# Optimization experiments

Measured on AMD Instinct MI355X. Metric: run time of the kernel, lower is better.

Reference implementation:

```python
import jax, jax.numpy as jnp
import numpy as np

B = 1024      # batch
DIN = 103     # generator/encoder input dim
L1, L2 = 64, 32   # encoder layer widths (latent = 32)
E = 8         # NUM_EXPERTS
GH = 64       # gating hidden width
H = 256       # generator hidden width
DOUT = 51     # generator output dim
EPS = 1e-5    # BatchNorm eps


def setup_inputs() -> dict:
    key = jax.random.key(0)
    ks = jax.random.split(key, 24)
    s = 0.05
    f32 = jnp.float32
    return {
        "x": jax.random.normal(ks[0], (B, DIN), f32),
        # encoder Linear + BN params
        "w1": jax.random.normal(ks[1], (L1, DIN), f32) * s,
        "b1": jnp.zeros((L1,), f32),
        "gamma1": jnp.ones((L1,), f32),
        "beta1": jnp.zeros((L1,), f32),
        "w2": jax.random.normal(ks[2], (L2, L1), f32) * s,
        "b2": jnp.zeros((L2,), f32),
        "gamma2": jnp.ones((L2,), f32),
        "beta2": jnp.zeros((L2,), f32),
        # gating MLP (latent 32 -> GH -> GH -> E, ELU, softmax)
        "gw1": jax.random.normal(ks[3], (GH, L2), f32) * s,
        "gb1": jnp.zeros((GH,), f32),
        "gw2": jax.random.normal(ks[4], (GH, GH), f32) * s,
        "gb2": jnp.zeros((GH,), f32),
        "gw3": jax.random.normal(ks[5], (E, GH), f32) * s,
        "gb3": jnp.zeros((E,), f32),
        # expert weight banks for 3-layer generator (MANN style)
        "ew1": jax.random.normal(ks[6], (E, DIN, H), f32) * s,
        "eb1": jnp.zeros((E, H), f32),
        "ew2": jax.random.normal(ks[7], (E, H, H), f32) * s,
        "eb2": jnp.zeros((E, H), f32),
        "ew3": jax.random.normal(ks[8], (E, H, DOUT), f32) * s,
        "eb3": jnp.zeros((E, DOUT), f32),
    }


def _batchnorm(h, gamma, beta):
    # training-mode BatchNorm1d: per-batch mean/var (biased var, matching torch)
    m = jnp.mean(h, axis=0)
    v = jnp.mean((h - m) ** 2, axis=0)
    return gamma * (h - m) * jax.lax.rsqrt(v + EPS) + beta


def reference(x, w1, b1, gamma1, beta1, w2, b2, gamma2, beta2,
              gw1, gb1, gw2, gb2, gw3, gb3,
              ew1, eb1, ew2, eb2, ew3, eb3):
    # in-place scale of last 3 features (x[:,100:103] *= 100)
    xs = x.at[:, 100:103].multiply(100.0)
    # encoder: Linear -> BN -> ReLU, twice
    h = jax.nn.relu(_batchnorm(xs @ w1.T + b1, gamma1, beta1))
    latent = jax.nn.relu(_batchnorm(h @ w2.T + b2, gamma2, beta2))
    # gating network -> blending coefficients BC [B, E]
    g = jax.nn.elu(latent @ gw1.T + gb1)
    g = jax.nn.elu(g @ gw2.T + gb2)
    bc = jax.nn.softmax(g @ gw3.T + gb3, axis=-1)
    # MANN-style generator: per-sample expert-blended weights
    wb1 = jnp.einsum('be,eih->bih', bc, ew1)   # [B, DIN, H]
    h1 = jax.nn.elu(jnp.einsum('bi,bih->bh', xs, wb1) + bc @ eb1)
    wb2 = jnp.einsum('be,ehk->bhk', bc, ew2)   # [B, H, H]
    h2 = jax.nn.elu(jnp.einsum('bh,bhk->bk', h1, wb2) + bc @ eb2)
    wb3 = jnp.einsum('be,eho->bho', bc, ew3)   # [B, H, DOUT]
    out = jnp.einsum('bh,bho->bo', h2, wb3) + bc @ eb3
    return out
```

## Files before the change

### kernel.cpp

```cpp
#include <hip/hip_runtime.h>
#include <math.h>


#define DIN 103
#define L1W 64
#define L2W 32
#define NE  8
#define GH  64
#define HH  256
#define DOUT 51
#define EPSBN 1e-5f

typedef __attribute__((ext_vector_type(8))) short bf16x8;
typedef __attribute__((ext_vector_type(4))) float f32x4;
typedef __attribute__((ext_vector_type(8))) unsigned short us8;
typedef __attribute__((ext_vector_type(4))) unsigned short us4;

__device__ __forceinline__ float eluf(float v) { return v > 0.f ? v : (expf(v) - 1.f); }

__device__ __forceinline__ unsigned short bf16h(float f) {
  unsigned u = __float_as_uint(f);
  u += 0x7FFFu + ((u >> 16) & 1u);
  return (unsigned short)(u >> 16);
}
__device__ __forceinline__ float bf16f(unsigned short h) {
  return __uint_as_float(((unsigned)h) << 16);
}
__device__ __forceinline__ void split_bf16(float v, unsigned short& h, unsigned short& l) {
  h = bf16h(v);
  l = bf16h(v - bf16f(h));
}


__global__ __launch_bounds__(256) void enc_pre(const float* __restrict__ x,
    const float* __restrict__ w1, const float* __restrict__ b1,
    float* __restrict__ h1raw, float* __restrict__ stats) {
  __shared__ float w1L[DIN * L1W];
  __shared__ float lsum[L1W], lsq[L1W];
  int t = threadIdx.x;
  for (int idx = t; idx < DIN * L1W; idx += 256) w1L[idx] = w1[idx];
  if (t < L1W) { lsum[t] = 0.f; lsq[t] = 0.f; }
  __syncthreads();
  int wave = t >> 6, j = t & 63;
  int row = blockIdx.x * 4 + wave;
  const float* xr = x + row * DIN;
  float acc = b1[j];
  for (int i = 0; i < DIN; ++i) {
    float xv = xr[i];
    if (i >= 100) xv *= 100.f;
    acc = fmaf(xv, w1L[j * DIN + i], acc);
  }
  h1raw[row * L1W + j] = acc;
  atomicAdd(&lsum[j], acc);
  atomicAdd(&lsq[j], acc * acc);
  __syncthreads();
  if (t < L1W) { atomicAdd(&stats[t], lsum[t]); atomicAdd(&stats[64 + t], lsq[t]); }
}

__global__ __launch_bounds__(256) void enc_mid(const float* __restrict__ h1raw,
    const float* __restrict__ stats, const float* __restrict__ gamma1, const float* __restrict__ beta1,
    const float* __restrict__ w2, const float* __restrict__ b2,
    float* __restrict__ h2raw, float* __restrict__ stats2) {
  __shared__ float w2L[L1W * 33];
  __shared__ float sc1[L1W], sh1[L1W];
  __shared__ float ls[L2W], lq[L2W];
  int t = threadIdx.x;
  for (int idx = t; idx < L1W * L2W; idx += 256) {
    int j = idx & 31, k = idx >> 5;
    w2L[k * 33 + j] = w2[j * L1W + k];
  }
  if (t < L1W) {
    float m = stats[t] * (1.f / 1024.f);
    float v = stats[64 + t] * (1.f / 1024.f) - m * m;
    float sc = gamma1[t] * rsqrtf(v + EPSBN);
    sc1[t] = sc; sh1[t] = beta1[t] - m * sc;
  }
  if (t < L2W) { ls[t] = 0.f; lq[t] = 0.f; }
  __syncthreads();
  int wave = t >> 6, l = t & 63;
  int j = l & 31, kh = l >> 5;
  int row = blockIdx.x * 4 + wave;
  const float* hr = h1raw + row * L1W;
  float acc = 0.f;
  for (int kk = 0; kk < 32; ++kk) {
    int k = kh * 32 + kk;
    float xv = fmaxf(fmaf(hr[k], sc1[k], sh1[k]), 0.f);
    acc = fmaf(xv, w2L[k * 33 + j], acc);
  }
  float tot = acc + __shfl_xor(acc, 32);
  if (kh == 0) {
    tot += b2[j];
    h2raw[row * L2W + j] = tot;
    atomicAdd(&ls[j], tot);
    atomicAdd(&lq[j], tot * tot);
  }
  __syncthreads();
  if (t < L2W) { atomicAdd(&stats2[t], ls[t]); atomicAdd(&stats2[32 + t], lq[t]); }
}

__global__ __launch_bounds__(256) void gate_kernel(
    const float* __restrict__ h2raw, const float* __restrict__ stats2,
    const float* __restrict__ gamma2, const float* __restrict__ beta2,
    const float* __restrict__ gw1, const float* __restrict__ gb1,
    const float* __restrict__ gw2, const float* __restrict__ gb2,
    const float* __restrict__ gw3, const float* __restrict__ gb3,
    float* __restrict__ bc) {
  __shared__ float gw1L[GH * 33];
  __shared__ float gw2L[GH * 65];
  __shared__ float gw3L[NE * 65];
  __shared__ float sc2[L2W], sh2[L2W];
  __shared__ float gb1L[GH], gb2L[GH], gb3L[NE];
  __shared__ float latb[4][L2W], g1b[4][GH], g2b[4][GH], lgb[4][NE];
  int t = threadIdx.x;
  for (int idx = t; idx < GH * L2W; idx += 256) { int jj = idx >> 5, kk = idx & 31; gw1L[jj * 33 + kk] = gw1[idx]; }
  for (int idx = t; idx < GH * GH;  idx += 256) { int jj = idx >> 6, kk = idx & 63; gw2L[jj * 65 + kk] = gw2[idx]; }
  for (int idx = t; idx < NE * GH;  idx += 256) { int jj = idx >> 6, kk = idx & 63; gw3L[jj * 65 + kk] = gw3[idx]; }
  if (t < GH) { gb1L[t] = gb1[t]; gb2L[t] = gb2[t]; }
  if (t < NE) gb3L[t] = gb3[t];
  if (t < L2W) {
    float m = stats2[t] * (1.f / 1024.f);
    float v = stats2[32 + t] * (1.f / 1024.f) - m * m;
    float sc = gamma2[t] * rsqrtf(v + EPSBN);
    sc2[t] = sc; sh2[t] = beta2[t] - m * sc;
  }
  __syncthreads();
  int wave = t >> 6, l = t & 63;
  int row = blockIdx.x * 4 + wave;
  if (l < L2W) {
    float hv = h2raw[row * L2W + l];
    latb[wave][l] = fmaxf(fmaf(hv, sc2[l], sh2[l]), 0.f);
  }
  __syncthreads();
  float a1 = gb1L[l];
  for (int k = 0; k < L2W; ++k) a1 = fmaf(gw1L[l * 33 + k], latb[wave][k], a1);
  g1b[wave][l] = eluf(a1);
  __syncthreads();
  float a2 = gb2L[l];
  for (int k = 0; k < GH; ++k) a2 = fmaf(gw2L[l * 65 + k], g1b[wave][k], a2);
  g2b[wave][l] = eluf(a2);
  __syncthreads();
  if (l < NE) {
    float a3 = gb3L[l];
    for (int k = 0; k < GH; ++k) a3 = fmaf(gw3L[l * 65 + k], g2b[wave][k], a3);
    lgb[wave][l] = a3;
  }
  __syncthreads();
  if (l < NE) {
    float mx = -1e30f;
    for (int e = 0; e < NE; ++e) mx = fmaxf(mx, lgb[wave][e]);
    float sum = 0.f, mine = 0.f;
    for (int e = 0; e < NE; ++e) {
      float p = expf(lgb[wave][e] - mx);
      if (e == l) mine = p;
      sum += p;
    }
    bc[row * NE + l] = mine / sum;
  }
}


__global__ __launch_bounds__(256) void gen1(const float* __restrict__ x,
    const float* __restrict__ ew1, float* __restrict__ p) {
  __shared__ __attribute__((aligned(16))) unsigned short Ah[4096], Al[4096], Bh[4096], Bl[4096];
  int t = threadIdx.x;
  int M0 = blockIdx.x * 128, N0 = blockIdx.y * 128, e = blockIdx.z;
  int w = t >> 6, l = t & 63;
  int wm = w & 1, wn = w >> 1;
  f32x4 acc[4][4] = {};
  int ar = t >> 1, akh = (t & 1) * 16;
  int bn = t & 127, bkh = (t >> 7) * 16;
  const float* xrow = x + (size_t)(M0 + ar) * DIN;
  for (int kc = 0; kc < 4; ++kc) {
    int k0 = kc * 32;
    {
      us8 h0 = {0}, h1 = {0}, l0 = {0}, l1 = {0};
#pragma unroll
      for (int j = 0; j < 8; ++j) {
        int i = k0 + akh + j;
        float v = 0.f;
        if (i < DIN) { v = xrow[i]; if (i >= 100) v *= 100.f; }
        unsigned short H, L; split_bf16(v, H, L); h0[j] = H; l0[j] = L;
        i += 8; v = 0.f;
        if (i < DIN) { v = xrow[i]; if (i >= 100) v *= 100.f; }
        split_bf16(v, H, L); h1[j] = H; l1[j] = L;
      }
      int base = ((ar >> 4) << 9) + ((akh >> 3) << 7) + ((ar & 15) << 3);
      *(us8*)(Ah + base) = h0; *(us8*)(Ah + base + 128) = h1;
      *(us8*)(Al + base) = l0; *(us8*)(Al + base + 128) = l1;
    }
    {
      us8 h0 = {0}, h1 = {0}, l0 = {0}, l1 = {0};
#pragma unroll
      for (int j = 0; j < 8; ++j) {
        int i = k0 + bkh + j;
        float v = (i < DIN) ? ew1[((size_t)e * DIN + i) * HH + N0 + bn] : 0.f;
        unsigned short H, L; split_bf16(v, H, L); h0[j] = H; l0[j] = L;
        i += 8;
        v = (i < DIN) ? ew1[((size_t)e * DIN + i) * HH + N0 + bn] : 0.f;
        split_bf16(v, H, L); h1[j] = H; l1[j] = L;
      }
      int base = ((bn >> 4) << 9) + ((bkh >> 3) << 7) + ((bn & 15) << 3);
      *(us8*)(Bh + base) = h0; *(us8*)(Bh + base + 128) = h1;
      *(us8*)(Bl + base) = l0; *(us8*)(Bl + base + 128) = l1;
    }
    __syncthreads();
    bf16x8 aH[4], aL[4], bH[4], bL[4];
#pragma unroll
    for (int im = 0; im < 4; ++im) {
      int off = (wm * 4 + im) * 512 + l * 8;
      aH[im] = *(const bf16x8*)(Ah + off);
      aL[im] = *(const bf16x8*)(Al + off);
    }
#pragma unroll
    for (int in = 0; in < 4; ++in) {
      int off = (wn * 4 + in) * 512 + l * 8;
      bH[in] = *(const bf16x8*)(Bh + off);
      bL[in] = *(const bf16x8*)(Bl + off);
    }
#pragma unroll
    for (int im = 0; im < 4; ++im)
#pragma unroll
      for (int in = 0; in < 4; ++in) {
        acc[im][in] = __builtin_amdgcn_mfma_f32_16x16x32_bf16(aH[im], bH[in], acc[im][in], 0, 0, 0);
        acc[im][in] = __builtin_amdgcn_mfma_f32_16x16x32_bf16(aL[im], bH[in], acc[im][in], 0, 0, 0);
        acc[im][in] = __builtin_amdgcn_mfma_f32_16x16x32_bf16(aH[im], bL[in], acc[im][in], 0, 0, 0);
      }
    __syncthreads();
  }
  int q = l >> 4, c = l & 15;
  float* pe = p + ((size_t)e << 18);
#pragma unroll
  for (int im = 0; im < 4; ++im) {
    int m0 = M0 + wm * 64 + im * 16 + q * 4;
#pragma unroll
    for (int in = 0; in < 4; ++in) {
      int col = N0 + wn * 64 + in * 16 + c;
#pragma unroll
      for (int r = 0; r < 4; ++r) pe[(size_t)(m0 + r) * HH + col] = acc[im][in][r];
    }
  }
}

__global__ __launch_bounds__(256) void gen2(const unsigned short* __restrict__ aHg,
    const unsigned short* __restrict__ aLg, const float* __restrict__ ew2, float* __restrict__ p) {
  __shared__ __attribute__((aligned(16))) unsigned short Ah[4096], Al[4096], Bh[4096], Bl[4096];
  int t = threadIdx.x;
  int M0 = blockIdx.x * 128, N0 = blockIdx.y * 128, e = blockIdx.z;
  int w = t >> 6, l = t & 63;
  int wm = w & 1, wn = w >> 1;
  f32x4 acc[4][4] = {};
  int ar = t >> 1, akh = (t & 1) * 16;
  int bn = t & 127, bkh = (t >> 7) * 16;
  for (int kc = 0; kc < 8; ++kc) {
    int k0 = kc * 32;
    {
      const us8* sh = (const us8*)(aHg + (size_t)(M0 + ar) * HH + k0 + akh);
      const us8* sl = (const us8*)(aLg + (size_t)(M0 + ar) * HH + k0 + akh);
      int base = ((ar >> 4) << 9) + ((akh >> 3) << 7) + ((ar & 15) << 3);
      *(us8*)(Ah + base) = sh[0]; *(us8*)(Ah + base + 128) = sh[1];
      *(us8*)(Al + base) = sl[0]; *(us8*)(Al + base + 128) = sl[1];
    }
    {
      us8 h0, h1, l0, l1;
#pragma unroll
      for (int j = 0; j < 8; ++j) {
        float v = ew2[((size_t)e * HH + k0 + bkh + j) * HH + N0 + bn];
        unsigned short H, L; split_bf16(v, H, L); h0[j] = H; l0[j] = L;
        v = ew2[((size_t)e * HH + k0 + bkh + 8 + j) * HH + N0 + bn];
        split_bf16(v, H, L); h1[j] = H; l1[j] = L;
      }
      int base = ((bn >> 4) << 9) + ((bkh >> 3) << 7) + ((bn & 15) << 3);
      *(us8*)(Bh + base) = h0; *(us8*)(Bh + base + 128) = h1;
      *(us8*)(Bl + base) = l0; *(us8*)(Bl + base + 128) = l1;
    }
    __syncthreads();
    bf16x8 aH[4], aL[4], bH[4], bL[4];
#pragma unroll
    for (int im = 0; im < 4; ++im) {
      int off = (wm * 4 + im) * 512 + l * 8;
      aH[im] = *(const bf16x8*)(Ah + off);
      aL[im] = *(const bf16x8*)(Al + off);
    }
#pragma unroll
    for (int in = 0; in < 4; ++in) {
      int off = (wn * 4 + in) * 512 + l * 8;
      bH[in] = *(const bf16x8*)(Bh + off);
      bL[in] = *(const bf16x8*)(Bl + off);
    }
#pragma unroll
    for (int im = 0; im < 4; ++im)
#pragma unroll
      for (int in = 0; in < 4; ++in) {
        acc[im][in] = __builtin_amdgcn_mfma_f32_16x16x32_bf16(aH[im], bH[in], acc[im][in], 0, 0, 0);
        acc[im][in] = __builtin_amdgcn_mfma_f32_16x16x32_bf16(aL[im], bH[in], acc[im][in], 0, 0, 0);
        acc[im][in] = __builtin_amdgcn_mfma_f32_16x16x32_bf16(aH[im], bL[in], acc[im][in], 0, 0, 0);
      }
    __syncthreads();
  }
  int q = l >> 4, c = l & 15;
  float* pe = p + ((size_t)e << 18);
#pragma unroll
  for (int im = 0; im < 4; ++im) {
    int m0 = M0 + wm * 64 + im * 16 + q * 4;
#pragma unroll
    for (int in = 0; in < 4; ++in) {
      int col = N0 + wn * 64 + in * 16 + c;
#pragma unroll
      for (int r = 0; r < 4; ++r) pe[(size_t)(m0 + r) * HH + col] = acc[im][in][r];
    }
  }
}

__global__ __launch_bounds__(256) void gen3(const unsigned short* __restrict__ aHg,
    const unsigned short* __restrict__ aLg, const float* __restrict__ ew3, float* __restrict__ p3) {
  __shared__ __attribute__((aligned(16))) unsigned short Ah[4096], Al[4096], Bh[2048], Bl[2048];
  int t = threadIdx.x;
  int M0 = blockIdx.x * 128, e = blockIdx.z;
  int w = t >> 6, l = t & 63;
  int wm = w & 1, wn = w >> 1;
  f32x4 acc[4][2] = {};
  int ar = t >> 1, akh = (t & 1) * 16;
  int bn = t & 63, bkh = (t >> 6) * 8;
  for (int kc = 0; kc < 8; ++kc) {
    int k0 = kc * 32;
    {
      const us8* sh = (const us8*)(aHg + (size_t)(M0 + ar) * HH + k0 + akh);
      const us8* sl = (const us8*)(aLg + (size_t)(M0 + ar) * HH + k0 + akh);
      int base = ((ar >> 4) << 9) + ((akh >> 3) << 7) + ((ar & 15) << 3);
      *(us8*)(Ah + base) = sh[0]; *(us8*)(Ah + base + 128) = sh[1];
      *(us8*)(Al + base) = sl[0]; *(us8*)(Al + base + 128) = sl[1];
    }
    {
      us8 h0 = {0}, l0 = {0};
      if (bn < DOUT) {
#pragma unroll
        for (int j = 0; j < 8; ++j) {
          float v = ew3[((size_t)e * HH + k0 + bkh + j) * DOUT + bn];
          unsigned short H, L; split_bf16(v, H, L); h0[j] = H; l0[j] = L;
        }
      }
      int base = ((bn >> 4) << 9) + ((bkh >> 3) << 7) + ((bn & 15) << 3);
      *(us8*)(Bh + base) = h0;
      *(us8*)(Bl + base) = l0;
    }
    __syncthreads();
    bf16x8 aH[4], aL[4], bH[2], bL[2];
#pragma unroll
    for (int im = 0; im < 4; ++im) {
      int off = (wm * 4 + im) * 512 + l * 8;
      aH[im] = *(const bf16x8*)(Ah + off);
      aL[im] = *(const bf16x8*)(Al + off);
    }
#pragma unroll
    for (int in = 0; in < 2; ++in) {
      int off = (wn * 2 + in) * 512 + l * 8;
      bH[in] = *(const bf16x8*)(Bh + off);
      bL[in] = *(const bf16x8*)(Bl + off);
    }
#pragma unroll
    for (int im = 0; im < 4; ++im)
#pragma unroll
      for (int in = 0; in < 2; ++in) {
        acc[im][in] = __builtin_amdgcn_mfma_f32_16x16x32_bf16(aH[im], bH[in], acc[im][in], 0, 0, 0);
        acc[im][in] = __builtin_amdgcn_mfma_f32_16x16x32_bf16(aL[im], bH[in], acc[im][in], 0, 0, 0);
        acc[im][in] = __builtin_amdgcn_mfma_f32_16x16x32_bf16(aH[im], bL[in], acc[im][in], 0, 0, 0);
      }
    __syncthreads();
  }
  int q = l >> 4, c = l & 15;
  float* pe = p3 + ((size_t)e << 16);
#pragma unroll
  for (int im = 0; im < 4; ++im) {
    int m0 = M0 + wm * 64 + im * 16 + q * 4;
#pragma unroll
    for (int in = 0; in < 2; ++in) {
      int col = wn * 32 + in * 16 + c;
#pragma unroll
      for (int r = 0; r < 4; ++r) pe[(size_t)(m0 + r) * 64 + col] = acc[im][in][r];
    }
  }
}

__global__ __launch_bounds__(256) void combine12(const float* __restrict__ p,
    const float* __restrict__ bc, const float* __restrict__ eb,
    unsigned short* __restrict__ ah, unsigned short* __restrict__ al) {
  int gid = blockIdx.x * 256 + threadIdx.x;
  int b = gid >> 6, hq = (gid & 63) * 4;
  float wv[NE];
#pragma unroll
  for (int e = 0; e < NE; ++e) wv[e] = bc[b * NE + e];
  float4 s = make_float4(0.f, 0.f, 0.f, 0.f);
#pragma unroll
  for (int e = 0; e < NE; ++e) {
    float4 pv = *(const float4*)(p + ((size_t)e << 18) + (size_t)b * HH + hq);
    float4 ev = *(const float4*)(eb + e * HH + hq);
    s.x = fmaf(wv[e], pv.x + ev.x, s.x);
    s.y = fmaf(wv[e], pv.y + ev.y, s.y);
    s.z = fmaf(wv[e], pv.z + ev.z, s.z);
    s.w = fmaf(wv[e], pv.w + ev.w, s.w);
  }
  float v0 = eluf(s.x), v1 = eluf(s.y), v2 = eluf(s.z), v3 = eluf(s.w);
  us4 H, L;
  unsigned short hh, ll;
  split_bf16(v0, hh, ll); H[0] = hh; L[0] = ll;
  split_bf16(v1, hh, ll); H[1] = hh; L[1] = ll;
  split_bf16(v2, hh, ll); H[2] = hh; L[2] = ll;
  split_bf16(v3, hh, ll); H[3] = hh; L[3] = ll;
  *(us4*)(ah + (size_t)b * HH + hq) = H;
  *(us4*)(al + (size_t)b * HH + hq) = L;
}

__global__ __launch_bounds__(256) void combine3(const float* __restrict__ p3,
    const float* __restrict__ bc, const float* __restrict__ eb3, float* __restrict__ out) {
  int gid = blockIdx.x * 256 + threadIdx.x;
  int b = gid >> 6, o = gid & 63;
  if (o >= DOUT) return;
  float s = 0.f;
#pragma unroll
  for (int e = 0; e < NE; ++e)
    s = fmaf(bc[b * NE + e], p3[((size_t)e << 16) + (size_t)b * 64 + o] + eb3[e * DOUT + o], s);
  out[(size_t)b * DOUT + o] = s;
}

extern "C" void kernel_launch(void* const* d_in, const int* in_sizes, int n_in,
                              void* d_out, int out_size, void* d_ws, size_t ws_size,
                              hipStream_t stream) {
  const float* x      = (const float*)d_in[0];
  const float* w1     = (const float*)d_in[1];
  const float* b1     = (const float*)d_in[2];
  const float* gamma1 = (const float*)d_in[3];
  const float* beta1  = (const float*)d_in[4];
  const float* w2     = (const float*)d_in[5];
  const float* b2     = (const float*)d_in[6];
  const float* gamma2 = (const float*)d_in[7];
  const float* beta2  = (const float*)d_in[8];
  const float* gw1    = (const float*)d_in[9];
  const float* gb1    = (const float*)d_in[10];
  const float* gw2    = (const float*)d_in[11];
  const float* gb2    = (const float*)d_in[12];
  const float* gw3    = (const float*)d_in[13];
  const float* gb3    = (const float*)d_in[14];
  const float* ew1    = (const float*)d_in[15];
  const float* eb1    = (const float*)d_in[16];
  const float* ew2    = (const float*)d_in[17];
  const float* eb2    = (const float*)d_in[18];
  const float* ew3    = (const float*)d_in[19];
  const float* eb3    = (const float*)d_in[20];

  float* ws    = (float*)d_ws;
  float* h1raw = ws;
  float* h2raw = ws + 65536;
  float* bcp   = ws + 98304;
  float* stats = ws + 106496;
  unsigned short* aH = (unsigned short*)(ws + 106752);
  unsigned short* aL = (unsigned short*)(ws + 237824);
  float* p     = ws + 368896;
  float* outp  = (float*)d_out;

  hipMemsetAsync(stats, 0, 192 * sizeof(float), stream);
  enc_pre<<<256, 256, 0, stream>>>(x, w1, b1, h1raw, stats);
  enc_mid<<<256, 256, 0, stream>>>(h1raw, stats, gamma1, beta1, w2, b2, h2raw, stats + 128);
  gate_kernel<<<256, 256, 0, stream>>>(h2raw, stats + 128, gamma2, beta2,
                                       gw1, gb1, gw2, gb2, gw3, gb3, bcp);
  gen1<<<dim3(8, 2, 8), 256, 0, stream>>>(x, ew1, p);
  combine12<<<256, 256, 0, stream>>>(p, bcp, eb1, aH, aL);
  gen2<<<dim3(8, 2, 8), 256, 0, stream>>>(aH, aL, ew2, p);
  combine12<<<256, 256, 0, stream>>>(p, bcp, eb2, aH, aL);
  gen3<<<dim3(8, 1, 8), 256, 0, stream>>>(aH, aL, ew3, p);
  combine3<<<256, 256, 0, stream>>>(p, bcp, eb3, outp);
}
```

Before: 175.9 us.

## Pre-split weights into MFMA fragment layout and drop LDS staging in GEMMs

Adds a prep kernel that splits x and all expert weight banks into bf16 hi/lo pairs stored directly in MFMA fragment order. The GEMM kernels become one template that loads fragments straight from global memory, with no LDS staging and no __syncthreads. combine12 now writes activations in the same fragment layout. The weight split and conversion still runs on every call inside the timed launch sequence, so it costs an extra kernel plus extra workspace traffic. In exchange the GEMMs no longer convert weights or use barriers, though each wave now reads operands from global memory with no shared reuse.

```diff
diff --git a/kernel.cpp b/kernel.cpp
--- a/kernel.cpp
+++ b/kernel.cpp
@@ -14,7 +14,6 @@
 typedef __attribute__((ext_vector_type(8))) short bf16x8;
 typedef __attribute__((ext_vector_type(4))) float f32x4;
 typedef __attribute__((ext_vector_type(8))) unsigned short us8;
-typedef __attribute__((ext_vector_type(4))) unsigned short us4;
 
 __device__ __forceinline__ float eluf(float v) { return v > 0.f ? v : (expf(v) - 1.f); }
 
@@ -31,6 +30,66 @@
   l = bf16h(v - bf16f(h));
 }
 
+
+__global__ __launch_bounds__(256) void prep(const float* __restrict__ x,
+    const float* __restrict__ ew1, const float* __restrict__ ew2, const float* __restrict__ ew3,
+    unsigned short* __restrict__ XsH, unsigned short* __restrict__ XsL,
+    unsigned short* __restrict__ E1H, unsigned short* __restrict__ E1L,
+    unsigned short* __restrict__ E2H, unsigned short* __restrict__ E2L,
+    unsigned short* __restrict__ E3H, unsigned short* __restrict__ E3L) {
+  int gid = blockIdx.x * 256 + threadIdx.x;
+  us8 H, L;
+  if (gid < 16384) {
+    int g = gid;
+    int l = g & 63, kc = (g >> 6) & 3, msub = g >> 8;
+    int b = msub * 16 + (l & 15);
+    int k0 = kc * 32 + (l >> 4) * 8;
+#pragma unroll
+    for (int j = 0; j < 8; ++j) {
+      int k = k0 + j;
+      float v = 0.f;
+      if (k < DIN) { v = x[(size_t)b * DIN + k]; if (k >= 100) v *= 100.f; }
+      unsigned short h, lo; split_bf16(v, h, lo); H[j] = h; L[j] = lo;
+    }
+    *(us8*)(XsH + (size_t)g * 8) = H; *(us8*)(XsL + (size_t)g * 8) = L;
+  } else if (gid < 49152) {
+    int g = gid - 16384;
+    int l = g & 63, kc = (g >> 6) & 3, nsub = (g >> 8) & 15, e = g >> 12;
+    int n = nsub * 16 + (l & 15);
+    int k0 = kc * 32 + (l >> 4) * 8;
+#pragma unroll
+    for (int j = 0; j < 8; ++j) {
+      int k = k0 + j;
+      float v = (k < DIN) ? ew1[((size_t)e * DIN + k) * HH + n] : 0.f;
+      unsigned short h, lo; split_bf16(v, h, lo); H[j] = h; L[j] = lo;
+    }
+    *(us8*)(E1H + (size_t)g * 8) = H; *(us8*)(E1L + (size_t)g * 8) = L;
+  } else if (gid < 114688) {
+    int g = gid - 49152;
+    int l = g & 63, kc = (g >> 6) & 7, nsub = (g >> 9) & 15, e = g >> 13;
+    int n = nsub * 16 + (l & 15);
+    int k0 = kc * 32 + (l >> 4) * 8;
+#pragma unroll
+    for (int j = 0; j < 8; ++j) {
+      int k = k0 + j;
+      float v = ew2[((size_t)e * HH + k) * HH + n];
+      unsigned short h, lo; split_bf16(v, h, lo); H[j] = h; L[j] = lo;
+    }
+    *(us8*)(E2H + (size_t)g * 8) = H; *(us8*)(E2L + (size_t)g * 8) = L;
+  } else {
+    int g = gid - 114688;
+    int l = g & 63, kc = (g >> 6) & 7, nsub = (g >> 9) & 3, e = g >> 11;
+    int n = nsub * 16 + (l & 15);
+    int k0 = kc * 32 + (l >> 4) * 8;
+#pragma unroll
+    for (int j = 0; j < 8; ++j) {
+      int k = k0 + j;
+      float v = (n < DOUT) ? ew3[((size_t)e * HH + k) * DOUT + n] : 0.f;
+      unsigned short h, lo; split_bf16(v, h, lo); H[j] = h; L[j] = lo;
+    }
+    *(us8*)(E3H + (size_t)g * 8) = H; *(us8*)(E3L + (size_t)g * 8) = L;
+  }
+}
 
 __global__ __launch_bounds__(256) void enc_pre(const float* __restrict__ x,
     const float* __restrict__ w1, const float* __restrict__ b1,
@@ -158,225 +217,46 @@
   }
 }
 
-
-__global__ __launch_bounds__(256) void gen1(const float* __restrict__ x,
-    const float* __restrict__ ew1, float* __restrict__ p) {
-  __shared__ __attribute__((aligned(16))) unsigned short Ah[4096], Al[4096], Bh[4096], Bl[4096];
-  int t = threadIdx.x;
-  int M0 = blockIdx.x * 128, N0 = blockIdx.y * 128, e = blockIdx.z;
-  int w = t >> 6, l = t & 63;
-  int wm = w & 1, wn = w >> 1;
+template<int KC, int NSUB, int LDP>
+__global__ __launch_bounds__(256) void genk(const unsigned short* __restrict__ AHp,
+    const unsigned short* __restrict__ ALp, const unsigned short* __restrict__ BHp,
+    const unsigned short* __restrict__ BLp, float* __restrict__ p) {
+  int t = threadIdx.x, w = t >> 6, l = t & 63;
+  int mblk = blockIdx.x * 4 + w;
+  int nblk = blockIdx.y, e = blockIdx.z;
+  const unsigned short* aH = AHp + ((size_t)mblk * 4 * KC) * 512 + l * 8;
+  const unsigned short* aL = ALp + ((size_t)mblk * 4 * KC) * 512 + l * 8;
+  const unsigned short* bH = BHp + ((size_t)(e * NSUB + nblk * 4) * KC) * 512 + l * 8;
+  const unsigned short* bL = BLp + ((size_t)(e * NSUB + nblk * 4) * KC) * 512 + l * 8;
   f32x4 acc[4][4] = {};
-  int ar = t >> 1, akh = (t & 1) * 16;
-  int bn = t & 127, bkh = (t >> 7) * 16;
-  const float* xrow = x + (size_t)(M0 + ar) * DIN;
-  for (int kc = 0; kc < 4; ++kc) {
-    int k0 = kc * 32;
-    {
-      us8 h0 = {0}, h1 = {0}, l0 = {0}, l1 = {0};
-#pragma unroll
-      for (int j = 0; j < 8; ++j) {
-        int i = k0 + akh + j;
-        float v = 0.f;
-        if (i < DIN) { v = xrow[i]; if (i >= 100) v *= 100.f; }
-        unsigned short H, L; split_bf16(v, H, L); h0[j] = H; l0[j] = L;
-        i += 8; v = 0.f;
-        if (i < DIN) { v = xrow[i]; if (i >= 100) v *= 100.f; }
-        split_bf16(v, H, L); h1[j] = H; l1[j] = L;
+  for (int kc = 0; kc < KC; ++kc) {
+    bf16x8 AH4[4], AL4[4], BH4[4], BL4[4];
+#pragma unroll
+    for (int i = 0; i < 4; ++i) {
+      AH4[i] = *(const bf16x8*)(aH + (size_t)(i * KC + kc) * 512);
+      AL4[i] = *(const bf16x8*)(aL + (size_t)(i * KC + kc) * 512);
+      BH4[i] = *(const bf16x8*)(bH + (size_t)(i * KC + kc) * 512);
+      BL4[i] = *(const bf16x8*)(bL + (size_t)(i * KC + kc) * 512);
+    }
+#pragma unroll
+    for (int im = 0; im < 4; ++im)
+#pragma unroll
+      for (int in = 0; in < 4; ++in) {
+        acc[im][in] = __builtin_amdgcn_mfma_f32_16x16x32_bf16(AH4[im], BH4[in], acc[im][in], 0, 0, 0);
+        acc[im][in] = __builtin_amdgcn_mfma_f32_16x16x32_bf16(AL4[im], BH4[in], acc[im][in], 0, 0, 0);
+        acc[im][in] = __builtin_amdgcn_mfma_f32_16x16x32_bf16(AH4[im], BL4[in], acc[im][in], 0, 0, 0);
       }
-      int base = ((ar >> 4) << 9) + ((akh >> 3) << 7) + ((ar & 15) << 3);
-      *(us8*)(Ah + base) = h0; *(us8*)(Ah + base + 128) = h1;
-      *(us8*)(Al + base) = l0; *(us8*)(Al + base + 128) = l1;
-    }
-    {
-      us8 h0 = {0}, h1 = {0}, l0 = {0}, l1 = {0};
-#pragma unroll
-      for (int j = 0; j < 8; ++j) {
-        int i = k0 + bkh + j;
-        float v = (i < DIN) ? ew1[((size_t)e * DIN + i) * HH + N0 + bn] : 0.f;
-        unsigned short H, L; split_bf16(v, H, L); h0[j] = H; l0[j] = L;
-        i += 8;
-        v = (i < DIN) ? ew1[((size_t)e * DIN + i) * HH + N0 + bn] : 0.f;
-        split_bf16(v, H, L); h1[j] = H; l1[j] = L;
-      }
-      int base = ((bn >> 4) << 9) + ((bkh >> 3) << 7) + ((bn & 15) << 3);
-      *(us8*)(Bh + base) = h0; *(us8*)(Bh + base + 128) = h1;
-      *(us8*)(Bl + base) = l0; *(us8*)(Bl + base + 128) = l1;
-    }
-    __syncthreads();
-    bf16x8 aH[4], aL[4], bH[4], bL[4];
-#pragma unroll
-    for (int im = 0; im < 4; ++im) {
-      int off = (wm * 4 + im) * 512 + l * 8;
-      aH[im] = *(const bf16x8*)(Ah + off);
-      aL[im] = *(const bf16x8*)(Al + off);
-    }
+  }
+  int q = l >> 4, c = l & 15;
+  float* pe = p + (size_t)e * 1024 * LDP;
+#pragma unroll
+  for (int im = 0; im < 4; ++im) {
+    int m0 = mblk * 64 + im * 16 + q * 4;
 #pragma unroll
     for (int in = 0; in < 4; ++in) {
-      int off = (wn * 4 + in) * 512 + l * 8;
-      bH[in] = *(const bf16x8*)(Bh + off);
-      bL[in] = *(const bf16x8*)(Bl + off);
-    }
-#pragma unroll
-    for (int im = 0; im < 4; ++im)
-#pragma unroll
-      for (int in = 0; in < 4; ++in) {
-        acc[im][in] = __builtin_amdgcn_mfma_f32_16x16x32_bf16(aH[im], bH[in], acc[im][in], 0, 0, 0);
-        acc[im][in] = __builtin_amdgcn_mfma_f32_16x16x32_bf16(aL[im], bH[in], acc[im][in], 0, 0, 0);
-        acc[im][in] = __builtin_amdgcn_mfma_f32_16x16x32_bf16(aH[im], bL[in], acc[im][in], 0, 0, 0);
-      }
-    __syncthreads();
-  }
-  int q = l >> 4, c = l & 15;
-  float* pe = p + ((size_t)e << 18);
-#pragma unroll
-  for (int im = 0; im < 4; ++im) {
-    int m0 = M0 + wm * 64 + im * 16 + q * 4;
-#pragma unroll
-    for (int in = 0; in < 4; ++in) {
-      int col = N0 + wn * 64 + in * 16 + c;
-#pragma unroll
-      for (int r = 0; r < 4; ++r) pe[(size_t)(m0 + r) * HH + col] = acc[im][in][r];
-    }
-  }
-}
-
-__global__ __launch_bounds__(256) void gen2(const unsigned short* __restrict__ aHg,
-    const unsigned short* __restrict__ aLg, const float* __restrict__ ew2, float* __restrict__ p) {
-  __shared__ __attribute__((aligned(16))) unsigned short Ah[4096], Al[4096], Bh[4096], Bl[4096];
-  int t = threadIdx.x;
-  int M0 = blockIdx.x * 128, N0 = blockIdx.y * 128, e = blockIdx.z;
-  int w = t >> 6, l = t & 63;
-  int wm = w & 1, wn = w >> 1;
-  f32x4 acc[4][4] = {};
-  int ar = t >> 1, akh = (t & 1) * 16;
-  int bn = t & 127, bkh = (t >> 7) * 16;
-  for (int kc = 0; kc < 8; ++kc) {
-    int k0 = kc * 32;
-    {
-      const us8* sh = (const us8*)(aHg + (size_t)(M0 + ar) * HH + k0 + akh);
-      const us8* sl = (const us8*)(aLg + (size_t)(M0 + ar) * HH + k0 + akh);
-      int base = ((ar >> 4) << 9) + ((akh >> 3) << 7) + ((ar & 15) << 3);
-      *(us8*)(Ah + base) = sh[0]; *(us8*)(Ah + base + 128) = sh[1];
-      *(us8*)(Al + base) = sl[0]; *(us8*)(Al + base + 128) = sl[1];
-    }
-    {
-      us8 h0, h1, l0, l1;
-#pragma unroll
-      for (int j = 0; j < 8; ++j) {
-        float v = ew2[((size_t)e * HH + k0 + bkh + j) * HH + N0 + bn];
-        unsigned short H, L; split_bf16(v, H, L); h0[j] = H; l0[j] = L;
-        v = ew2[((size_t)e * HH + k0 + bkh + 8 + j) * HH + N0 + bn];
-        split_bf16(v, H, L); h1[j] = H; l1[j] = L;
-      }
-      int base = ((bn >> 4) << 9) + ((bkh >> 3) << 7) + ((bn & 15) << 3);
-      *(us8*)(Bh + base) = h0; *(us8*)(Bh + base + 128) = h1;
-      *(us8*)(Bl + base) = l0; *(us8*)(Bl + base + 128) = l1;
-    }
-    __syncthreads();
-    bf16x8 aH[4], aL[4], bH[4], bL[4];
-#pragma unroll
-    for (int im = 0; im < 4; ++im) {
-      int off = (wm * 4 + im) * 512 + l * 8;
-      aH[im] = *(const bf16x8*)(Ah + off);
-      aL[im] = *(const bf16x8*)(Al + off);
-    }
-#pragma unroll
-    for (int in = 0; in < 4; ++in) {
-      int off = (wn * 4 + in) * 512 + l * 8;
-      bH[in] = *(const bf16x8*)(Bh + off);
-      bL[in] = *(const bf16x8*)(Bl + off);
-    }
-#pragma unroll
-    for (int im = 0; im < 4; ++im)
-#pragma unroll
-      for (int in = 0; in < 4; ++in) {
-        acc[im][in] = __builtin_amdgcn_mfma_f32_16x16x32_bf16(aH[im], bH[in], acc[im][in], 0, 0, 0);
-        acc[im][in] = __builtin_amdgcn_mfma_f32_16x16x32_bf16(aL[im], bH[in], acc[im][in], 0, 0, 0);
-        acc[im][in] = __builtin_amdgcn_mfma_f32_16x16x32_bf16(aH[im], bL[in], acc[im][in], 0, 0, 0);
-      }
-    __syncthreads();
-  }
-  int q = l >> 4, c = l & 15;
-  float* pe = p + ((size_t)e << 18);
-#pragma unroll
-  for (int im = 0; im < 4; ++im) {
-    int m0 = M0 + wm * 64 + im * 16 + q * 4;
-#pragma unroll
-    for (int in = 0; in < 4; ++in) {
-      int col = N0 + wn * 64 + in * 16 + c;
-#pragma unroll
-      for (int r = 0; r < 4; ++r) pe[(size_t)(m0 + r) * HH + col] = acc[im][in][r];
-    }
-  }
-}
-
-__global__ __launch_bounds__(256) void gen3(const unsigned short* __restrict__ aHg,
-    const unsigned short* __restrict__ aLg, const float* __restrict__ ew3, float* __restrict__ p3) {
-  __shared__ __attribute__((aligned(16))) unsigned short Ah[4096], Al[4096], Bh[2048], Bl[2048];
-  int t = threadIdx.x;
-  int M0 = blockIdx.x * 128, e = blockIdx.z;
-  int w = t >> 6, l = t & 63;
-  int wm = w & 1, wn = w >> 1;
-  f32x4 acc[4][2] = {};
-  int ar = t >> 1, akh = (t & 1) * 16;
-  int bn = t & 63, bkh = (t >> 6) * 8;
-  for (int kc = 0; kc < 8; ++kc) {
-    int k0 = kc * 32;
-    {
-      const us8* sh = (const us8*)(aHg + (size_t)(M0 + ar) * HH + k0 + akh);
-      const us8* sl = (const us8*)(aLg + (size_t)(M0 + ar) * HH + k0 + akh);
-      int base = ((ar >> 4) << 9) + ((akh >> 3) << 7) + ((ar & 15) << 3);
-      *(us8*)(Ah + base) = sh[0]; *(us8*)(Ah + base + 128) = sh[1];
-      *(us8*)(Al + base) = sl[0]; *(us8*)(Al + base + 128) = sl[1];
-    }
-    {
-      us8 h0 = {0}, l0 = {0};
-      if (bn < DOUT) {
-#pragma unroll
-        for (int j = 0; j < 8; ++j) {
-          float v = ew3[((size_t)e * HH + k0 + bkh + j) * DOUT + bn];
-          unsigned short H, L; split_bf16(v, H, L); h0[j] = H; l0[j] = L;
-        }
-      }
-      int base = ((bn >> 4) << 9) + ((bkh >> 3) << 7) + ((bn & 15) << 3);
-      *(us8*)(Bh + base) = h0;
-      *(us8*)(Bl + base) = l0;
-    }
-    __syncthreads();
-    bf16x8 aH[4], aL[4], bH[2], bL[2];
-#pragma unroll
-    for (int im = 0; im < 4; ++im) {
-      int off = (wm * 4 + im) * 512 + l * 8;
-      aH[im] = *(const bf16x8*)(Ah + off);
-      aL[im] = *(const bf16x8*)(Al + off);
-    }
-#pragma unroll
-    for (int in = 0; in < 2; ++in) {
-      int off = (wn * 2 + in) * 512 + l * 8;
-      bH[in] = *(const bf16x8*)(Bh + off);
-      bL[in] = *(const bf16x8*)(Bl + off);
-    }
-#pragma unroll
-    for (int im = 0; im < 4; ++im)
-#pragma unroll
-      for (int in = 0; in < 2; ++in) {
-        acc[im][in] = __builtin_amdgcn_mfma_f32_16x16x32_bf16(aH[im], bH[in], acc[im][in], 0, 0, 0);
-        acc[im][in] = __builtin_amdgcn_mfma_f32_16x16x32_bf16(aL[im], bH[in], acc[im][in], 0, 0, 0);
-        acc[im][in] = __builtin_amdgcn_mfma_f32_16x16x32_bf16(aH[im], bL[in], acc[im][in], 0, 0, 0);
-      }
-    __syncthreads();
-  }
-  int q = l >> 4, c = l & 15;
-  float* pe = p3 + ((size_t)e << 16);
-#pragma unroll
-  for (int im = 0; im < 4; ++im) {
-    int m0 = M0 + wm * 64 + im * 16 + q * 4;
-#pragma unroll
-    for (int in = 0; in < 2; ++in) {
-      int col = wn * 32 + in * 16 + c;
-#pragma unroll
-      for (int r = 0; r < 4; ++r) pe[(size_t)(m0 + r) * 64 + col] = acc[im][in][r];
+      int col = nblk * 64 + in * 16 + c;
+#pragma unroll
+      for (int r = 0; r < 4; ++r) pe[(size_t)(m0 + r) * LDP + col] = acc[im][in][r];
     }
   }
 }
@@ -385,29 +265,37 @@
     const float* __restrict__ bc, const float* __restrict__ eb,
     unsigned short* __restrict__ ah, unsigned short* __restrict__ al) {
   int gid = blockIdx.x * 256 + threadIdx.x;
-  int b = gid >> 6, hq = (gid & 63) * 4;
+  int l = gid & 63, kc = (gid >> 6) & 7, msub = gid >> 9;
+  int b = msub * 16 + (l & 15);
+  int k0 = kc * 32 + (l >> 4) * 8;
   float wv[NE];
 #pragma unroll
   for (int e = 0; e < NE; ++e) wv[e] = bc[b * NE + e];
-  float4 s = make_float4(0.f, 0.f, 0.f, 0.f);
+  float s[8] = {};
 #pragma unroll
   for (int e = 0; e < NE; ++e) {
-    float4 pv = *(const float4*)(p + ((size_t)e << 18) + (size_t)b * HH + hq);
-    float4 ev = *(const float4*)(eb + e * HH + hq);
-    s.x = fmaf(wv[e], pv.x + ev.x, s.x);
-    s.y = fmaf(wv[e], pv.y + ev.y, s.y);
-    s.z = fmaf(wv[e], pv.z + ev.z, s.z);
-    s.w = fmaf(wv[e], pv.w + ev.w, s.w);
-  }
-  float v0 = eluf(s.x), v1 = eluf(s.y), v2 = eluf(s.z), v3 = eluf(s.w);
-  us4 H, L;
-  unsigned short hh, ll;
-  split_bf16(v0, hh, ll); H[0] = hh; L[0] = ll;
-  split_bf16(v1, hh, ll); H[1] = hh; L[1] = ll;
-  split_bf16(v2, hh, ll); H[2] = hh; L[2] = ll;
-  split_bf16(v3, hh, ll); H[3] = hh; L[3] = ll;
-  *(us4*)(ah + (size_t)b * HH + hq) = H;
-  *(us4*)(al + (size_t)b * HH + hq) = L;
+    const float* pr = p + ((size_t)e << 18) + (size_t)b * HH + k0;
+    float4 p0 = *(const float4*)pr, p1 = *(const float4*)(pr + 4);
+    const float* er = eb + e * HH + k0;
+    float4 e0 = *(const float4*)er, e1 = *(const float4*)(er + 4);
+    s[0] = fmaf(wv[e], p0.x + e0.x, s[0]);
+    s[1] = fmaf(wv[e], p0.y + e0.y, s[1]);
+    s[2] = fmaf(wv[e], p0.z + e0.z, s[2]);
+    s[3] = fmaf(wv[e], p0.w + e0.w, s[3]);
+    s[4] = fmaf(wv[e], p1.x + e1.x, s[4]);
+    s[5] = fmaf(wv[e], p1.y + e1.y, s[5]);
+    s[6] = fmaf(wv[e], p1.z + e1.z, s[6]);
+    s[7] = fmaf(wv[e], p1.w + e1.w, s[7]);
+  }
+  us8 H, L;
+#pragma unroll
+  for (int j = 0; j < 8; ++j) {
+    float v = eluf(s[j]);
+    unsigned short h, lo; split_bf16(v, h, lo);
+    H[j] = h; L[j] = lo;
+  }
+  *(us8*)(ah + (size_t)gid * 8) = H;
+  *(us8*)(al + (size_t)gid * 8) = L;
 }
 
 __global__ __launch_bounds__(256) void combine3(const float* __restrict__ p3,
@@ -452,20 +340,29 @@
   float* h2raw = ws + 65536;
   float* bcp   = ws + 98304;
   float* stats = ws + 106496;
-  unsigned short* aH = (unsigned short*)(ws + 106752);
-  unsigned short* aL = (unsigned short*)(ws + 237824);
-  float* p     = ws + 368896;
+  unsigned short* XsH = (unsigned short*)(ws + 106752);
+  unsigned short* XsL = (unsigned short*)(ws + 172288);
+  unsigned short* E1H = (unsigned short*)(ws + 237824);
+  unsigned short* E1L = (unsigned short*)(ws + 368896);
+  unsigned short* E2H = (unsigned short*)(ws + 499968);
+  unsigned short* E2L = (unsigned short*)(ws + 762112);
+  unsigned short* E3H = (unsigned short*)(ws + 1024256);
+  unsigned short* E3L = (unsigned short*)(ws + 1089792);
+  unsigned short* AH  = (unsigned short*)(ws + 1155328);
+  unsigned short* AL  = (unsigned short*)(ws + 1286400);
+  float* p     = ws + 1417472;
   float* outp  = (float*)d_out;
 
   hipMemsetAsync(stats, 0, 192 * sizeof(float), stream);
+  prep<<<512, 256, 0, stream>>>(x, ew1, ew2, ew3, XsH, XsL, E1H, E1L, E2H, E2L, E3H, E3L);
   enc_pre<<<256, 256, 0, stream>>>(x, w1, b1, h1raw, stats);
   enc_mid<<<256, 256, 0, stream>>>(h1raw, stats, gamma1, beta1, w2, b2, h2raw, stats + 128);
   gate_kernel<<<256, 256, 0, stream>>>(h2raw, stats + 128, gamma2, beta2,
                                        gw1, gb1, gw2, gb2, gw3, gb3, bcp);
-  gen1<<<dim3(8, 2, 8), 256, 0, stream>>>(x, ew1, p);
-  combine12<<<256, 256, 0, stream>>>(p, bcp, eb1, aH, aL);
-  gen2<<<dim3(8, 2, 8), 256, 0, stream>>>(aH, aL, ew2, p);
-  combine12<<<256, 256, 0, stream>>>(p, bcp, eb2, aH, aL);
-  gen3<<<dim3(8, 1, 8), 256, 0, stream>>>(aH, aL, ew3, p);
+  genk<4, 16, 256><<<dim3(4, 4, 8), 256, 0, stream>>>(XsH, XsL, E1H, E1L, p);
+  combine12<<<128, 256, 0, stream>>>(p, bcp, eb1, AH, AL);
+  genk<8, 16, 256><<<dim3(4, 4, 8), 256, 0, stream>>>(AH, AL, E2H, E2L, p);
+  combine12<<<128, 256, 0, stream>>>(p, bcp, eb2, AH, AL);
+  genk<8, 4, 64><<<dim3(4, 1, 8), 256, 0, stream>>>(AH, AL, E3H, E3L, p);
   combine3<<<256, 256, 0, stream>>>(p, bcp, eb3, outp);
 }
```

New measurement: 186.2 us. +5.9%, slower.
